# Kernel tuning notes

Measured on AMD Instinct MI355X. Metric: run time of the kernel, lower is better.

## Reference

```python
import jax, jax.numpy as jnp
import numpy as np

H, I, E, K = 1024, 2048, 8, 2
B, T = 4, 2048


def setup_inputs() -> dict:
    key = jax.random.key(0)
    k0, k1, k2, k3 = jax.random.split(key, 4)
    x = jax.random.normal(k0, (B, T, H), dtype=jnp.float32)
    Wg = jax.random.normal(k1, (E, H), dtype=jnp.float32) * 0.02   # gate: Linear(H->E), weight [E,H]
    W1 = jax.random.normal(k2, (E, I, H), dtype=jnp.float32) * 0.02  # per-expert fc1 weights [I,H]
    W2 = jax.random.normal(k3, (E, H, I), dtype=jnp.float32) * 0.02  # per-expert fc2 weights [H,I]
    return {"x": x, "Wg": Wg, "W1": W1, "W2": W2, "top_k": K}


def reference(x, Wg, W1, W2, top_k):
    b, t, h = x.shape
    xf = x.reshape(-1, h)                                  # [N,H], N=B*T
    gate_probs = jax.nn.softmax(xf @ Wg.T, axis=-1)        # [N,E]
    topk_vals, topk_idx = jax.lax.top_k(gate_probs, top_k) # [N,k]
    # Dense all-expert SiLU-MLP (faithful to the original dense MoE):
    hid = jax.nn.silu(jnp.einsum('nh,eih->nei', xf, W1))   # [N,E,I]
    all_outs = jnp.einsum('nei,ehi->neh', hid, W2)         # [N,E,H]
    topk_outs = jnp.take_along_axis(all_outs, topk_idx[:, :, None], axis=1)  # [N,k,H]
    weighted = (topk_outs * topk_vals[:, :, None]).sum(axis=1)               # [N,H]
    return weighted.reshape(b, t, h)
```

## Files before the change

kernel.cpp:

```cpp
#include <hip/hip_runtime.h>
#include <hip/hip_bf16.h>

#define HH 1024
#define II 2048
#define EE 8
#define NTOK 8192
#define NPAIR (NTOK * 2)

typedef __attribute__((ext_vector_type(8))) short bf16x8;
typedef __attribute__((ext_vector_type(4))) float f32x4;
typedef unsigned int u32;

__device__ __forceinline__ ushort f2bf(float f) {
    union { float f; unsigned u; } v; v.f = f;
    unsigned r = v.u + 0x7fffu + ((v.u >> 16) & 1u);
    return (ushort)(r >> 16);
}

__device__ __forceinline__ void gload16(const void* g, void* l) {
    __builtin_amdgcn_global_load_lds((const __attribute__((address_space(1))) u32*)g,
                                     (__attribute__((address_space(3))) u32*)l, 16, 0, 0);
}

__device__ __forceinline__ int expert_off(const int* __restrict__ counts, int e) {
    int off = 0;
#pragma unroll
    for (int i = 0; i < EE; i++) off += (i < e) ? counts[i] : 0;
    return off;
}

__global__ __launch_bounds__(256) void cvtw_kernel(
    const float* __restrict__ W1, const float* __restrict__ W2,
    ushort* __restrict__ W1b, ushort* __restrict__ W2b)
{
    const int N1 = EE * II * HH / 4;
    const int i = blockIdx.x * 256 + threadIdx.x;
    const float4 f = (i < N1) ? ((const float4*)W1)[i] : ((const float4*)W2)[i - N1];
    union { ushort h[4]; uint2 u; } pk;
    pk.h[0] = f2bf(f.x); pk.h[1] = f2bf(f.y); pk.h[2] = f2bf(f.z); pk.h[3] = f2bf(f.w);
    if (i < N1) ((uint2*)W1b)[i] = pk.u;
    else        ((uint2*)W2b)[i - N1] = pk.u;
}

__global__ __launch_bounds__(256) void gate_kernel(
    const float* __restrict__ x, const float* __restrict__ Wg,
    int* __restrict__ counts, int* __restrict__ tki, float* __restrict__ tkv,
    ushort* __restrict__ xb)
{
    __shared__ int hist[EE];
    const int tid = threadIdx.x;
    if (tid < EE) hist[tid] = 0;
    __syncthreads();

    const int w = tid >> 6, lane = tid & 63;

#pragma unroll 1
    for (int t = 0; t < 8; t++) {
        const int n = blockIdx.x * 32 + w * 8 + t;
        const float* xr = x + (size_t)n * HH;
        float4 xv[4];
#pragma unroll
        for (int c = 0; c < 4; c++) xv[c] = *(const float4*)(xr + c * 256 + lane * 4);

#pragma unroll
        for (int c = 0; c < 4; c++) {
            union { ushort h[4]; uint2 u; } pk;
            pk.h[0] = f2bf(xv[c].x); pk.h[1] = f2bf(xv[c].y);
            pk.h[2] = f2bf(xv[c].z); pk.h[3] = f2bf(xv[c].w);
            *(uint2*)(xb + (size_t)n * HH + c * 256 + lane * 4) = pk.u;
        }

        float dot[EE];
#pragma unroll
        for (int e = 0; e < EE; e++) {
            float s = 0.f;
#pragma unroll
            for (int c = 0; c < 4; c++) {
                const float4 wv = *(const float4*)(Wg + e * HH + c * 256 + lane * 4);
                s += xv[c].x * wv.x + xv[c].y * wv.y + xv[c].z * wv.z + xv[c].w * wv.w;
            }
            for (int off = 32; off > 0; off >>= 1) s += __shfl_down(s, off);
            dot[e] = s;
        }
        if (lane == 0) {
            float m = dot[0];
#pragma unroll
            for (int e = 1; e < EE; e++) m = fmaxf(m, dot[e]);
            float p[EE]; float sum = 0.f;
#pragma unroll
            for (int e = 0; e < EE; e++) { p[e] = __expf(dot[e] - m); sum += p[e]; }
            const float inv = 1.f / sum;
            int i0 = 0; float v0 = p[0];
#pragma unroll
            for (int e = 1; e < EE; e++) if (p[e] > v0) { v0 = p[e]; i0 = e; }
            int i1 = -1; float v1 = -1.f;
#pragma unroll
            for (int e = 0; e < EE; e++) if (e != i0 && p[e] > v1) { v1 = p[e]; i1 = e; }
            tki[n * 2 + 0] = i0; tkv[n * 2 + 0] = v0 * inv;
            tki[n * 2 + 1] = i1; tkv[n * 2 + 1] = v1 * inv;
            atomicAdd(&hist[i0], 1);
            atomicAdd(&hist[i1], 1);
        }
    }
    __syncthreads();
    if (tid < EE) atomicAdd(&counts[tid], hist[tid]);
}

__global__ __launch_bounds__(256) void scatter_kernel(
    const int* __restrict__ tki, const float* __restrict__ tkv,
    const int* __restrict__ counts,
    int* __restrict__ cursor, int* __restrict__ stok, float* __restrict__ sval,
    int* __restrict__ pslot)
{
    __shared__ int hist[EE];
    __shared__ int base[EE];
    const int tid = threadIdx.x;
    const int id = blockIdx.x * 256 + tid;
    if (tid < EE) hist[tid] = 0;
    __syncthreads();
    const int e = tki[id];
    const int loc = atomicAdd(&hist[e], 1);
    __syncthreads();
    if (tid < EE) {
        int off = 0;
        for (int i = 0; i < tid; i++) off += counts[i];
        base[tid] = off + atomicAdd(&cursor[tid], hist[tid]);
    }
    __syncthreads();
    const int p = base[e] + loc;
    stok[p] = id >> 1;
    sval[p] = tkv[id];
    pslot[id] = p;
}

__global__ __launch_bounds__(256) void gather_kernel(
    const float* __restrict__ tmp, const float* __restrict__ tkv,
    const int* __restrict__ pslot, float* __restrict__ out)
{
    const int t = blockIdx.x;
    const int tid = threadIdx.x;
    const int p0 = pslot[2 * t], p1 = pslot[2 * t + 1];
    const float v0 = tkv[2 * t], v1 = tkv[2 * t + 1];
    const float4 a = ((const float4*)(tmp + (size_t)p0 * HH))[tid];
    const float4 b = ((const float4*)(tmp + (size_t)p1 * HH))[tid];
    float4 o;
    o.x = v0 * a.x + v1 * b.x;
    o.y = v0 * a.y + v1 * b.y;
    o.z = v0 * a.z + v1 * b.z;
    o.w = v0 * a.w + v1 * b.w;
    ((float4*)(out + (size_t)t * HH))[tid] = o;
}

template <bool PRE>
__global__ __launch_bounds__(256) void fc1_kernel(
    const float* __restrict__ x, const ushort* __restrict__ xb,
    const float* __restrict__ W1, const ushort* __restrict__ W1b,
    const int* __restrict__ counts,
    const int* __restrict__ stok, ushort* __restrict__ hid)
{
    const int e = blockIdx.z;
    const int cnt = counts[e];
    const int row0 = blockIdx.y * 128;
    if (row0 >= cnt) return;
    const int off = expert_off(counts, e);
    const int col0 = blockIdx.x * 128;

    __shared__ __align__(16) ushort As[128 * 64];
    __shared__ __align__(16) ushort Bs[128 * 64];

    const int tid = threadIdx.x;
    const int w = tid >> 6, lane = tid & 63;
    const int quad = lane >> 4, l16 = lane & 15;
    const int wm = (w >> 1) * 64, wn = (w & 1) * 64;
    const int l7 = l16 & 7;

    f32x4 acc[4][4];
#pragma unroll
    for (int mi = 0; mi < 4; mi++)
#pragma unroll
        for (int ni = 0; ni < 4; ni++) acc[mi][ni] = f32x4{0.f, 0.f, 0.f, 0.f};

    const int sub = lane >> 3;
    const int chk = lane & 7;
    const int gchk = chk ^ sub;
    int tokA[4];
    const int fr = tid >> 1;
    const int fc = (tid & 1) * 32;
    int tokF = 0;
    if (PRE) {
#pragma unroll
        for (int i = 0; i < 4; i++) {
            int r = row0 + (w * 4 + i) * 8 + sub;
            if (r >= cnt) r = cnt - 1;
            tokA[i] = stok[off + r];
        }
    } else {
        int r = row0 + fr;
        if (r >= cnt) r = cnt - 1;
        tokF = stok[off + r];
    }

    if (PRE) {
#pragma unroll 1
        for (int it = 0; it < HH / 64; it++) {
            const int k0 = it * 64;
            __syncthreads();
#pragma unroll
            for (int i = 0; i < 4; i++) {
                const ushort* gA = xb + (size_t)tokA[i] * HH + k0 + gchk * 8;
                gload16(gA, &As[(w * 4 + i) * 512]);
                const ushort* gB = W1b + ((size_t)e * II + col0 + (w * 4 + i) * 8 + sub) * HH + k0 + gchk * 8;
                gload16(gB, &Bs[(w * 4 + i) * 512]);
            }
            __syncthreads();
#pragma unroll
            for (int kk = 0; kk < 2; kk++) {
                const int pos = ((kk * 4 + quad) ^ l7) * 8;
                bf16x8 af[4], bb[4];
#pragma unroll
                for (int mi = 0; mi < 4; mi++)
                    af[mi] = *(const bf16x8*)&As[(wm + mi * 16 + l16) * 64 + pos];
#pragma unroll
                for (int ni = 0; ni < 4; ni++)
                    bb[ni] = *(const bf16x8*)&Bs[(wn + ni * 16 + l16) * 64 + pos];
#pragma unroll
                for (int mi = 0; mi < 4; mi++)
#pragma unroll
                    for (int ni = 0; ni < 4; ni++)
                        acc[mi][ni] = __builtin_amdgcn_mfma_f32_16x16x32_bf16(af[mi], bb[ni], acc[mi][ni], 0, 0, 0);
            }
        }
    } else {
#pragma unroll 1
        for (int k0 = 0; k0 < HH; k0 += 64) {
            __syncthreads();
#pragma unroll
            for (int c = 0; c < 32; c += 4) {
                const int u = fc + c;
                const int sw = ((u >> 3) ^ (fr & 7)) * 8 + (u & 7);
                const float4 f = *(const float4*)(x + (size_t)tokF * HH + k0 + u);
                union { ushort h[4]; uint2 u2; } pk;
                pk.h[0] = f2bf(f.x); pk.h[1] = f2bf(f.y); pk.h[2] = f2bf(f.z); pk.h[3] = f2bf(f.w);
                *(uint2*)&As[fr * 64 + sw] = pk.u2;
                const float4 g = *(const float4*)(W1 + ((size_t)e * II + col0 + fr) * HH + k0 + u);
                pk.h[0] = f2bf(g.x); pk.h[1] = f2bf(g.y); pk.h[2] = f2bf(g.z); pk.h[3] = f2bf(g.w);
                *(uint2*)&Bs[fr * 64 + sw] = pk.u2;
            }
            __syncthreads();
#pragma unroll
            for (int kk = 0; kk < 2; kk++) {
                const int pos = ((kk * 4 + quad) ^ l7) * 8;
                bf16x8 af[4], bb[4];
#pragma unroll
                for (int mi = 0; mi < 4; mi++)
                    af[mi] = *(const bf16x8*)&As[(wm + mi * 16 + l16) * 64 + pos];
#pragma unroll
                for (int ni = 0; ni < 4; ni++)
                    bb[ni] = *(const bf16x8*)&Bs[(wn + ni * 16 + l16) * 64 + pos];
#pragma unroll
                for (int mi = 0; mi < 4; mi++)
#pragma unroll
                    for (int ni = 0; ni < 4; ni++)
                        acc[mi][ni] = __builtin_amdgcn_mfma_f32_16x16x32_bf16(af[mi], bb[ni], acc[mi][ni], 0, 0, 0);
            }
        }
    }

    const int cnt_rem = cnt - row0;
#pragma unroll
    for (int mi = 0; mi < 4; mi++) {
#pragma unroll
        for (int j = 0; j < 4; j++) {
            const int r = wm + mi * 16 + quad * 4 + j;
            if (r < cnt_rem) {
                ushort* hrow = hid + (size_t)(off + row0 + r) * II + col0 + wn + l16;
#pragma unroll
                for (int ni = 0; ni < 4; ni++) {
                    const float v = acc[mi][ni][j];
                    const float s = v / (1.f + __expf(-v));
                    hrow[ni * 16] = f2bf(s);
                }
            }
        }
    }
}

template <bool PRE, bool TMP>
__global__ __launch_bounds__(256) void fc2_kernel(
    const ushort* __restrict__ hid,
    const float* __restrict__ W2, const ushort* __restrict__ W2b,
    const int* __restrict__ counts,
    const int* __restrict__ stok, const float* __restrict__ sval,
    float* __restrict__ tmp, float* __restrict__ out)
{
    const int e = blockIdx.z;
    const int cnt = counts[e];
    const int row0 = blockIdx.y * 128;
    if (row0 >= cnt) return;
    const int off = expert_off(counts, e);
    const int col0 = blockIdx.x * 128;

    __shared__ __align__(16) ushort As[128 * 64];
    __shared__ __align__(16) ushort Bs[128 * 64];

    const int tid = threadIdx.x;
    const int w = tid >> 6, lane = tid & 63;
    const int quad = lane >> 4, l16 = lane & 15;
    const int wm = (w >> 1) * 64, wn = (w & 1) * 64;
    const int l7 = l16 & 7;

    f32x4 acc[4][4];
#pragma unroll
    for (int mi = 0; mi < 4; mi++)
#pragma unroll
        for (int ni = 0; ni < 4; ni++) acc[mi][ni] = f32x4{0.f, 0.f, 0.f, 0.f};

    const int sub = lane >> 3;
    const int chk = lane & 7;
    const int gchk = chk ^ sub;
    size_t slotA[4];
#pragma unroll
    for (int i = 0; i < 4; i++) {
        int s = off + row0 + (w * 4 + i) * 8 + sub;
        if (s > NPAIR - 1) s = NPAIR - 1;
        slotA[i] = (size_t)s;
    }
    const int fr = tid >> 1;
    const int fc = (tid & 1) * 32;

    if (PRE) {
#pragma unroll 1
        for (int it = 0; it < II / 64; it++) {
            const int k0 = it * 64;
            __syncthreads();
#pragma unroll
            for (int i = 0; i < 4; i++) {
                const ushort* gA = hid + slotA[i] * II + k0 + gchk * 8;
                gload16(gA, &As[(w * 4 + i) * 512]);
                const ushort* gB = W2b + ((size_t)e * HH + col0 + (w * 4 + i) * 8 + sub) * II + k0 + gchk * 8;
                gload16(gB, &Bs[(w * 4 + i) * 512]);
            }
            __syncthreads();
#pragma unroll
            for (int kk = 0; kk < 2; kk++) {
                const int pos = ((kk * 4 + quad) ^ l7) * 8;
                bf16x8 af[4], bb[4];
#pragma unroll
                for (int mi = 0; mi < 4; mi++)
                    af[mi] = *(const bf16x8*)&As[(wm + mi * 16 + l16) * 64 + pos];
#pragma unroll
                for (int ni = 0; ni < 4; ni++)
                    bb[ni] = *(const bf16x8*)&Bs[(wn + ni * 16 + l16) * 64 + pos];
#pragma unroll
                for (int mi = 0; mi < 4; mi++)
#pragma unroll
                    for (int ni = 0; ni < 4; ni++)
                        acc[mi][ni] = __builtin_amdgcn_mfma_f32_16x16x32_bf16(af[mi], bb[ni], acc[mi][ni], 0, 0, 0);
            }
        }
    } else {
#pragma unroll 1
        for (int k0 = 0; k0 < II; k0 += 64) {
            __syncthreads();
#pragma unroll
            for (int i = 0; i < 4; i++) {
                const ushort* gA = hid + slotA[i] * II + k0 + gchk * 8;
                gload16(gA, &As[(w * 4 + i) * 512]);
            }
#pragma unroll
            for (int c = 0; c < 32; c += 4) {
                const int u = fc + c;
                const int sw = ((u >> 3) ^ (fr & 7)) * 8 + (u & 7);
                const float4 g = *(const float4*)(W2 + ((size_t)e * HH + col0 + fr) * II + k0 + u);
                union { ushort h[4]; uint2 u2; } pk;
                pk.h[0] = f2bf(g.x); pk.h[1] = f2bf(g.y); pk.h[2] = f2bf(g.z); pk.h[3] = f2bf(g.w);
                *(uint2*)&Bs[fr * 64 + sw] = pk.u2;
            }
            __syncthreads();
#pragma unroll
            for (int kk = 0; kk < 2; kk++) {
                const int pos = ((kk * 4 + quad) ^ l7) * 8;
                bf16x8 af[4], bb[4];
#pragma unroll
                for (int mi = 0; mi < 4; mi++)
                    af[mi] = *(const bf16x8*)&As[(wm + mi * 16 + l16) * 64 + pos];
#pragma unroll
                for (int ni = 0; ni < 4; ni++)
                    bb[ni] = *(const bf16x8*)&Bs[(wn + ni * 16 + l16) * 64 + pos];
#pragma unroll
                for (int mi = 0; mi < 4; mi++)
#pragma unroll
                    for (int ni = 0; ni < 4; ni++)
                        acc[mi][ni] = __builtin_amdgcn_mfma_f32_16x16x32_bf16(af[mi], bb[ni], acc[mi][ni], 0, 0, 0);
            }
        }
    }

    const int cnt_rem = cnt - row0;
#pragma unroll
    for (int mi = 0; mi < 4; mi++) {
#pragma unroll
        for (int j = 0; j < 4; j++) {
            const int r = wm + mi * 16 + quad * 4 + j;
            if (r < cnt_rem) {
                const int p = off + row0 + r;
                if (TMP) {
                    float* orow = tmp + (size_t)p * HH + col0 + wn + l16;
#pragma unroll
                    for (int ni = 0; ni < 4; ni++)
                        orow[ni * 16] = acc[mi][ni][j];
                } else {
                    const int token = stok[p];
                    const float val = sval[p];
                    float* orow = out + (size_t)token * HH + col0 + wn + l16;
#pragma unroll
                    for (int ni = 0; ni < 4; ni++)
                        atomicAdd(&orow[ni * 16], val * acc[mi][ni][j]);
                }
            }
        }
    }
}

extern "C" void kernel_launch(void* const* d_in, const int* in_sizes, int n_in,
                              void* d_out, int out_size, void* d_ws, size_t ws_size,
                              hipStream_t stream) {
    const float* x  = (const float*)d_in[0];
    const float* Wg = (const float*)d_in[1];
    const float* W1 = (const float*)d_in[2];
    const float* W2 = (const float*)d_in[3];
    float* out = (float*)d_out;

    char* wsb = (char*)d_ws;
    int*    counts = (int*)(wsb + 0);
    int*    cursor = (int*)(wsb + 64);
    int*    tki    = (int*)(wsb + 256);
    float*  tkv    = (float*)(wsb + 256 + 65536);
    int*    stok   = (int*)(wsb + 256 + 2 * 65536);
    float*  sval   = (float*)(wsb + 256 + 3 * 65536);
    int*    pslot  = (int*)(wsb + 256 + 4 * 65536);
    const size_t HDR = 256 + 5 * 65536;
    ushort* hid    = (ushort*)(wsb + HDR);
    ushort* W1b    = (ushort*)(wsb + HDR + 67108864ull);
    ushort* W2b    = (ushort*)(wsb + HDR + 100663296ull);
    ushort* xb     = (ushort*)(wsb + HDR + 134217728ull);
    float*  tmp    = (float*)(wsb + HDR + 150994944ull);
    const size_t REQ1 = HDR + 150994944ull;
    const size_t REQ2 = REQ1 + 67108864ull;
    const bool pre  = ws_size >= REQ1;
    const bool tmpp = ws_size >= REQ2;

    hipMemsetAsync(wsb, 0, 256, stream);
    if (!tmpp)
        hipMemsetAsync(d_out, 0, (size_t)out_size * sizeof(float), stream);

    gate_kernel<<<NTOK / 32, 256, 0, stream>>>(x, Wg, counts, tki, tkv, xb);
    scatter_kernel<<<NPAIR / 256, 256, 0, stream>>>(tki, tkv, counts, cursor, stok, sval, pslot);

    if (pre) {
        cvtw_kernel<<<(2 * EE * II * HH / 4) / 256, 256, 0, stream>>>(W1, W2, W1b, W2b);
        fc1_kernel<true><<<dim3(II / 128, NPAIR / 128, EE), 256, 0, stream>>>(x, xb, W1, W1b, counts, stok, hid);
        if (tmpp) {
            fc2_kernel<true, true><<<dim3(HH / 128, NPAIR / 128, EE), 256, 0, stream>>>(hid, W2, W2b, counts, stok, sval, tmp, out);
            gather_kernel<<<NTOK, 256, 0, stream>>>(tmp, tkv, pslot, out);
        } else {
            fc2_kernel<true, false><<<dim3(HH / 128, NPAIR / 128, EE), 256, 0, stream>>>(hid, W2, W2b, counts, stok, sval, tmp, out);
        }
    } else {
        fc1_kernel<false><<<dim3(II / 128, NPAIR / 128, EE), 256, 0, stream>>>(x, xb, W1, W1b, counts, stok, hid);
        fc2_kernel<false, false><<<dim3(HH / 128, NPAIR / 128, EE), 256, 0, stream>>>(hid, W2, W2b, counts, stok, sval, tmp, out);
    }
}
```

Measured before the change: 407.0 us.

## Flatten grouped-GEMM grid into packed tile list with XCD-aware remapping

The fc1/fc2 grids change from a 3D grid (cols × all 128 row-tiles × experts), where most blocks exit early, to a 1D grid sized for at most 136 occupied row-tiles. Each block decodes its expert and row tile by walking cumulative per-expert tile counts. Block ids are remapped so consecutive logical tiles land on the same XCD, which should improve L2 reuse of weight tiles. The gate kernel also moves to one token per wavefront with more blocks. MAXT assumes the total of ceil(count/128) across experts stays within 136.

```diff
diff --git a/kernel.cpp b/kernel.cpp
--- a/kernel.cpp
+++ b/kernel.cpp
@@ -6,6 +6,7 @@
 #define EE 8
 #define NTOK 8192
 #define NPAIR (NTOK * 2)
+#define MAXT 136
 
 typedef __attribute__((ext_vector_type(8))) short bf16x8;
 typedef __attribute__((ext_vector_type(4))) float f32x4;
@@ -22,11 +23,36 @@
                                      (__attribute__((address_space(3))) u32*)l, 16, 0, 0);
 }
 
-__device__ __forceinline__ int expert_off(const int* __restrict__ counts, int e) {
-    int off = 0;
-#pragma unroll
-    for (int i = 0; i < EE; i++) off += (i < e) ? counts[i] : 0;
-    return off;
+template <int COLS>
+__device__ __forceinline__ bool tile_map(const int* __restrict__ counts,
+                                         int& e, int& cnt, int& row0, int& off, int& col0)
+{
+    const int orig = blockIdx.x;
+    const int nwg  = COLS * MAXT;
+    const int qq = nwg >> 3, rr = nwg & 7;
+    const int xcd = orig & 7, lid = orig >> 3;
+    const int logical = (xcd < rr ? xcd * (qq + 1) : rr * (qq + 1) + (xcd - rr) * qq) + lid;
+    const int ft   = logical / COLS;
+    const int colt = logical - ft * COLS;
+    int carr[EE];
+#pragma unroll
+    for (int i = 0; i < EE; i++) carr[i] = counts[i];
+    e = -1; off = 0;
+    int rt = 0, t0 = 0;
+#pragma unroll
+    for (int i = 0; i < EE; i++) {
+        const int nt = (carr[i] + 127) >> 7;
+        if (e < 0) {
+            if (ft < t0 + nt) { e = i; rt = ft - t0; }
+            else off += carr[i];
+        }
+        t0 += nt;
+    }
+    if (e < 0) return false;
+    cnt  = carr[e];
+    row0 = rt * 128;
+    col0 = colt * 128;
+    return true;
 }
 
 __global__ __launch_bounds__(256) void cvtw_kernel(
@@ -53,54 +79,50 @@
     __syncthreads();
 
     const int w = tid >> 6, lane = tid & 63;
-
-#pragma unroll 1
-    for (int t = 0; t < 8; t++) {
-        const int n = blockIdx.x * 32 + w * 8 + t;
-        const float* xr = x + (size_t)n * HH;
-        float4 xv[4];
-#pragma unroll
-        for (int c = 0; c < 4; c++) xv[c] = *(const float4*)(xr + c * 256 + lane * 4);
-
+    const int n = blockIdx.x * 4 + w;
+    const float* xr = x + (size_t)n * HH;
+    float4 xv[4];
+#pragma unroll
+    for (int c = 0; c < 4; c++) xv[c] = *(const float4*)(xr + c * 256 + lane * 4);
+
+#pragma unroll
+    for (int c = 0; c < 4; c++) {
+        union { ushort h[4]; uint2 u; } pk;
+        pk.h[0] = f2bf(xv[c].x); pk.h[1] = f2bf(xv[c].y);
+        pk.h[2] = f2bf(xv[c].z); pk.h[3] = f2bf(xv[c].w);
+        *(uint2*)(xb + (size_t)n * HH + c * 256 + lane * 4) = pk.u;
+    }
+
+    float dot[EE];
+#pragma unroll
+    for (int e = 0; e < EE; e++) {
+        float s = 0.f;
 #pragma unroll
         for (int c = 0; c < 4; c++) {
-            union { ushort h[4]; uint2 u; } pk;
-            pk.h[0] = f2bf(xv[c].x); pk.h[1] = f2bf(xv[c].y);
-            pk.h[2] = f2bf(xv[c].z); pk.h[3] = f2bf(xv[c].w);
-            *(uint2*)(xb + (size_t)n * HH + c * 256 + lane * 4) = pk.u;
-        }
-
-        float dot[EE];
-#pragma unroll
-        for (int e = 0; e < EE; e++) {
-            float s = 0.f;
-#pragma unroll
-            for (int c = 0; c < 4; c++) {
-                const float4 wv = *(const float4*)(Wg + e * HH + c * 256 + lane * 4);
-                s += xv[c].x * wv.x + xv[c].y * wv.y + xv[c].z * wv.z + xv[c].w * wv.w;
-            }
-            for (int off = 32; off > 0; off >>= 1) s += __shfl_down(s, off);
-            dot[e] = s;
-        }
-        if (lane == 0) {
-            float m = dot[0];
-#pragma unroll
-            for (int e = 1; e < EE; e++) m = fmaxf(m, dot[e]);
-            float p[EE]; float sum = 0.f;
-#pragma unroll
-            for (int e = 0; e < EE; e++) { p[e] = __expf(dot[e] - m); sum += p[e]; }
-            const float inv = 1.f / sum;
-            int i0 = 0; float v0 = p[0];
-#pragma unroll
-            for (int e = 1; e < EE; e++) if (p[e] > v0) { v0 = p[e]; i0 = e; }
-            int i1 = -1; float v1 = -1.f;
-#pragma unroll
-            for (int e = 0; e < EE; e++) if (e != i0 && p[e] > v1) { v1 = p[e]; i1 = e; }
-            tki[n * 2 + 0] = i0; tkv[n * 2 + 0] = v0 * inv;
-            tki[n * 2 + 1] = i1; tkv[n * 2 + 1] = v1 * inv;
-            atomicAdd(&hist[i0], 1);
-            atomicAdd(&hist[i1], 1);
-        }
+            const float4 wv = *(const float4*)(Wg + e * HH + c * 256 + lane * 4);
+            s += xv[c].x * wv.x + xv[c].y * wv.y + xv[c].z * wv.z + xv[c].w * wv.w;
+        }
+        for (int off = 32; off > 0; off >>= 1) s += __shfl_down(s, off);
+        dot[e] = s;
+    }
+    if (lane == 0) {
+        float m = dot[0];
+#pragma unroll
+        for (int e = 1; e < EE; e++) m = fmaxf(m, dot[e]);
+        float p[EE]; float sum = 0.f;
+#pragma unroll
+        for (int e = 0; e < EE; e++) { p[e] = __expf(dot[e] - m); sum += p[e]; }
+        const float inv = 1.f / sum;
+        int i0 = 0; float v0 = p[0];
+#pragma unroll
+        for (int e = 1; e < EE; e++) if (p[e] > v0) { v0 = p[e]; i0 = e; }
+        int i1 = -1; float v1 = -1.f;
+#pragma unroll
+        for (int e = 0; e < EE; e++) if (e != i0 && p[e] > v1) { v1 = p[e]; i1 = e; }
+        tki[n * 2 + 0] = i0; tkv[n * 2 + 0] = v0 * inv;
+        tki[n * 2 + 1] = i1; tkv[n * 2 + 1] = v1 * inv;
+        atomicAdd(&hist[i0], 1);
+        atomicAdd(&hist[i1], 1);
     }
     __syncthreads();
     if (tid < EE) atomicAdd(&counts[tid], hist[tid]);
@@ -158,12 +180,8 @@
     const int* __restrict__ counts,
     const int* __restrict__ stok, ushort* __restrict__ hid)
 {
-    const int e = blockIdx.z;
-    const int cnt = counts[e];
-    const int row0 = blockIdx.y * 128;
-    if (row0 >= cnt) return;
-    const int off = expert_off(counts, e);
-    const int col0 = blockIdx.x * 128;
+    int e, cnt, row0, off, col0;
+    if (!tile_map<II / 128>(counts, e, cnt, row0, off, col0)) return;
 
     __shared__ __align__(16) ushort As[128 * 64];
     __shared__ __align__(16) ushort Bs[128 * 64];
@@ -293,12 +311,8 @@
     const int* __restrict__ stok, const float* __restrict__ sval,
     float* __restrict__ tmp, float* __restrict__ out)
 {
-    const int e = blockIdx.z;
-    const int cnt = counts[e];
-    const int row0 = blockIdx.y * 128;
-    if (row0 >= cnt) return;
-    const int off = expert_off(counts, e);
-    const int col0 = blockIdx.x * 128;
+    int e, cnt, row0, off, col0;
+    if (!tile_map<HH / 128>(counts, e, cnt, row0, off, col0)) return;
 
     __shared__ __align__(16) ushort As[128 * 64];
     __shared__ __align__(16) ushort Bs[128 * 64];
@@ -454,20 +468,22 @@
     if (!tmpp)
         hipMemsetAsync(d_out, 0, (size_t)out_size * sizeof(float), stream);
 
-    gate_kernel<<<NTOK / 32, 256, 0, stream>>>(x, Wg, counts, tki, tkv, xb);
+    gate_kernel<<<NTOK / 4, 256, 0, stream>>>(x, Wg, counts, tki, tkv, xb);
     scatter_kernel<<<NPAIR / 256, 256, 0, stream>>>(tki, tkv, counts, cursor, stok, sval, pslot);
 
+    const int G1 = (II / 128) * MAXT;
+    const int G2 = (HH / 128) * MAXT;
     if (pre) {
         cvtw_kernel<<<(2 * EE * II * HH / 4) / 256, 256, 0, stream>>>(W1, W2, W1b, W2b);
-        fc1_kernel<true><<<dim3(II / 128, NPAIR / 128, EE), 256, 0, stream>>>(x, xb, W1, W1b, counts, stok, hid);
+        fc1_kernel<true><<<G1, 256, 0, stream>>>(x, xb, W1, W1b, counts, stok, hid);
         if (tmpp) {
-            fc2_kernel<true, true><<<dim3(HH / 128, NPAIR / 128, EE), 256, 0, stream>>>(hid, W2, W2b, counts, stok, sval, tmp, out);
+            fc2_kernel<true, true><<<G2, 256, 0, stream>>>(hid, W2, W2b, counts, stok, sval, tmp, out);
             gather_kernel<<<NTOK, 256, 0, stream>>>(tmp, tkv, pslot, out);
         } else {
-            fc2_kernel<true, false><<<dim3(HH / 128, NPAIR / 128, EE), 256, 0, stream>>>(hid, W2, W2b, counts, stok, sval, tmp, out);
+            fc2_kernel<true, false><<<G2, 256, 0, stream>>>(hid, W2, W2b, counts, stok, sval, tmp, out);
         }
     } else {
-        fc1_kernel<false><<<dim3(II / 128, NPAIR / 128, EE), 256, 0, stream>>>(x, xb, W1, W1b, counts, stok, hid);
-        fc2_kernel<false, false><<<dim3(HH / 128, NPAIR / 128, EE), 256, 0, stream>>>(hid, W2, W2b, counts, stok, sval, tmp, out);
-    }
-}
+        fc1_kernel<false><<<G1, 256, 0, stream>>>(x, xb, W1, W1b, counts, stok, hid);
+        fc2_kernel<false, false><<<G2, 256, 0, stream>>>(hid, W2, W2b, counts, stok, sval, tmp, out);
+    }
+}
```

Result: no change. 414.4 us (+1.8%).
